# Performance work log

Measured on AMD Instinct MI355X. Metric: run time of the kernel, lower is better.

The kernel has to match this reference:

```python
import jax, jax.numpy as jnp
import numpy as np

EMBED_DIM = 1024
N_HEADS = 16
DK = EMBED_DIM // N_HEADS


def setup_inputs() -> dict:
    key = jax.random.key(0)
    ks = jax.random.split(key, 9)
    s = 1.0 / np.sqrt(EMBED_DIM)
    d = EMBED_DIM
    return {
        "x": jax.random.normal(ks[0], (2, 2048, d), dtype=jnp.float32),
        "Wq": jax.random.uniform(ks[1], (d, d), jnp.float32, -s, s),
        "bq": jax.random.uniform(ks[2], (d,), jnp.float32, -s, s),
        "Wk": jax.random.uniform(ks[3], (d, d), jnp.float32, -s, s),
        "bk": jax.random.uniform(ks[4], (d,), jnp.float32, -s, s),
        "Wv": jax.random.uniform(ks[5], (d, d), jnp.float32, -s, s),
        "bv": jax.random.uniform(ks[6], (d,), jnp.float32, -s, s),
        "Wo": jax.random.uniform(ks[7], (d, d), jnp.float32, -s, s),
        "bo": jax.random.uniform(ks[8], (d,), jnp.float32, -s, s),
    }


def reference(x, Wq, bq, Wk, bk, Wv, bv, Wo, bo):
    B, S, D = x.shape
    H, dk = N_HEADS, DK
    # QKV projections
    q = (x @ Wq + bq).reshape(B, S, H, dk).transpose(0, 2, 1, 3)  # [B,H,S,dk]
    k = (x @ Wk + bk).reshape(B, S, H, dk).transpose(0, 2, 1, 3)
    v = (x @ Wv + bv).reshape(B, S, H, dk).transpose(0, 2, 1, 3)
    # scaled dot-product attention with full score matrix (faithful to source)
    scores = jnp.einsum("bhqd,bhkd->bhqk", q, k) / jnp.sqrt(jnp.float32(dk))
    attn = jax.nn.softmax(scores, axis=-1)
    out = jnp.einsum("bhqk,bhkd->bhqd", attn, v)  # [B,H,S,dk]
    out = out.transpose(0, 2, 1, 3).reshape(B, S, D)
    return out @ Wo + bo
```

## Files before the change

### kernel.cpp

```cpp
#include <hip/hip_runtime.h>

typedef unsigned short u16;
typedef unsigned int u32;
typedef __attribute__((ext_vector_type(8))) short short8;
typedef __attribute__((ext_vector_type(4))) float float4v;

struct alignas(8) U16x4 { u16 x, y, z, w; };

__device__ __forceinline__ u16 f2b(float f) {
    union { float f; unsigned int u; } v; v.f = f;
    unsigned int r = (v.u >> 16) & 1u;
    v.u += 0x7fffu + r;
    return (u16)(v.u >> 16);
}

__device__ __forceinline__ float b2f(u16 u) {
    union { unsigned int u; float f; } v; v.u = ((u32)u) << 16; return v.f;
}

__device__ __forceinline__ void gld16(const u16* g, u16* l) {
    __builtin_amdgcn_global_load_lds(
        (const __attribute__((address_space(1))) void*)g,
        (__attribute__((address_space(3))) void*)l, 16, 0, 0);
}

__device__ __forceinline__ short8 frag8(const u16* base, int row, int cg) {
    return *(const short8*)(base + row * 64 + ((cg ^ (row & 7)) << 3));
}

__global__ __launch_bounds__(256) void prep_kernel(
    const float* __restrict__ x, const float* __restrict__ W0,
    const float* __restrict__ W1, const float* __restrict__ W2,
    const float* __restrict__ W3, u16* __restrict__ xb,
    u16* __restrict__ T0, u16* __restrict__ T1,
    u16* __restrict__ T2, u16* __restrict__ T3) {
    __shared__ float tile[32][33];
    int id = blockIdx.x;
    if (id < 4096) {
        size_t i = ((size_t)id * 256 + threadIdx.x) * 4;
        float4 v = *(const float4*)(x + i);
        U16x4 o;
        o.x = f2b(v.x); o.y = f2b(v.y); o.z = f2b(v.z); o.w = f2b(v.w);
        *(U16x4*)(xb + i) = o;
        return;
    }
    int r = id - 4096;
    int z = r >> 10, tl = r & 1023;
    const float* W = (z == 0) ? W0 : (z == 1) ? W1 : (z == 2) ? W2 : W3;
    u16* T = (z == 0) ? T0 : (z == 1) ? T1 : (z == 2) ? T2 : T3;
    int t = threadIdx.x;
    int tx = t & 31, ty = t >> 5;
    int bn = (tl & 31) * 32, bk = (tl >> 5) * 32;
#pragma unroll
    for (int p = 0; p < 4; ++p) {
        int k = ty + p * 8;
        tile[k][tx] = W[(size_t)(bk + k) * 1024 + bn + tx];
    }
    __syncthreads();
#pragma unroll
    for (int p = 0; p < 4; ++p) {
        int n = ty + p * 8;
        T[(size_t)(bn + n) * 1024 + bk + tx] = f2b(tile[tx][n]);
    }
}

__global__ __launch_bounds__(512, 2) void qkv_kernel(
    const u16* __restrict__ X,
    const u16* __restrict__ WqT, const u16* __restrict__ WkT, const u16* __restrict__ WvT,
    const float* __restrict__ bq, const float* __restrict__ bk, const float* __restrict__ bv,
    u16* __restrict__ Qo, u16* __restrict__ Ko, u16* __restrict__ VTo) {
    __shared__ __align__(16) u16 As[128 * 64];
    __shared__ __align__(16) u16 Bs[3][128 * 64];
    int id = blockIdx.x;
    int m = (id & 7) | (((id >> 3) & 3) << 3);
    int n = id >> 5;
    int t = threadIdx.x;
    int m0 = m * 128, n0 = n * 128;
    int lane = t & 63, wid = t >> 6;
    int wr = wid >> 2, wc = wid & 3;
    int l16 = lane & 15, quad = lane >> 4;
    int rl = lane >> 3, cs = lane & 7;

    int tileid = wid >> 1, half = wid & 1;
    const u16* gsrc = (tileid == 0) ? X : (tileid == 1) ? WqT
                     : (tileid == 2) ? WkT : WvT;
    int gbase = (tileid == 0) ? m0 : n0;
    u16* ldst = (tileid == 0) ? As : &Bs[tileid - 1][0];

    float4v acc[3][4][2];
    float4v zero4 = {0.f, 0.f, 0.f, 0.f};
#pragma unroll
    for (int z = 0; z < 3; ++z)
#pragma unroll
        for (int i = 0; i < 4; ++i)
#pragma unroll
            for (int j = 0; j < 2; ++j) acc[z][i][j] = zero4;

    for (int k0 = 0; k0 < 1024; k0 += 64) {
        __syncthreads();
#pragma unroll
        for (int p = 0; p < 8; ++p) {
            int q = half * 8 + p;
            int row = q * 8 + rl;
            int c = cs ^ (row & 7);
            gld16(gsrc + (size_t)(gbase + row) * 1024 + k0 + c * 8, ldst + q * 512);
        }
        __syncthreads();
#pragma unroll
        for (int ks = 0; ks < 64; ks += 32) {
            int cg = (ks >> 3) + quad;
            short8 af[4];
#pragma unroll
            for (int i = 0; i < 4; ++i)
                af[i] = frag8(As, wr * 64 + i * 16 + l16, cg);
#pragma unroll
            for (int z = 0; z < 3; ++z) {
                short8 bf[2];
#pragma unroll
                for (int j = 0; j < 2; ++j)
                    bf[j] = frag8(&Bs[z][0], wc * 32 + j * 16 + l16, cg);
#pragma unroll
                for (int i = 0; i < 4; ++i)
#pragma unroll
                    for (int j = 0; j < 2; ++j)
                        acc[z][i][j] = __builtin_amdgcn_mfma_f32_16x16x32_bf16(
                            af[i], bf[j], acc[z][i][j], 0, 0, 0);
            }
        }
    }

    const float QSCALE = 0.18033688011112042f;
#pragma unroll
    for (int j = 0; j < 2; ++j) {
        int n1 = n0 + wc * 32 + j * 16 + l16;
        float bql = bq[n1], bkl = bk[n1], bvl = bv[n1];
#pragma unroll
        for (int i = 0; i < 4; ++i) {
            int mbase = m0 + wr * 64 + i * 16 + quad * 4;
#pragma unroll
            for (int r = 0; r < 4; ++r) {
                Qo[(size_t)(mbase + r) * 1024 + n1] =
                    f2b((acc[0][i][j][r] + bql) * QSCALE);
                Ko[(size_t)(mbase + r) * 1024 + n1] =
                    f2b(acc[1][i][j][r] + bkl);
            }
            int bidx = mbase >> 11, s = mbase & 2047;
            size_t base =
                ((size_t)((bidx * 16 + (n1 >> 6)) * 64 + (n1 & 63))) * 2048 + s;
            U16x4 pk;
            pk.x = f2b(acc[2][i][j][0] + bvl);
            pk.y = f2b(acc[2][i][j][1] + bvl);
            pk.z = f2b(acc[2][i][j][2] + bvl);
            pk.w = f2b(acc[2][i][j][3] + bvl);
            *(U16x4*)(VTo + base) = pk;
        }
    }
}

__global__ __launch_bounds__(256) void oproj_kernel(const u16* __restrict__ X,
                                                    const u16* __restrict__ WoT,
                                                    const float* __restrict__ bias,
                                                    float* __restrict__ out) {
    __shared__ __align__(16) u16 As[64 * 64];
    __shared__ __align__(16) u16 Bs[128 * 64];
    int id = blockIdx.x;
    int m = (id & 7) | (((id >> 3) & 7) << 3);
    int n = id >> 6;
    int t = threadIdx.x;
    int m0 = m * 64, n0 = n * 128;
    int lane = t & 63, wid = t >> 6;
    int l16 = lane & 15, quad = lane >> 4;
    int rl = lane >> 3, cs = lane & 7;

    float4v acc[4][2];
    float4v zero4 = {0.f, 0.f, 0.f, 0.f};
#pragma unroll
    for (int i = 0; i < 4; ++i)
#pragma unroll
        for (int j = 0; j < 2; ++j) acc[i][j] = zero4;

    for (int k0 = 0; k0 < 1024; k0 += 64) {
        __syncthreads();
#pragma unroll
        for (int p = 0; p < 2; ++p) {
            int blk = wid * 2 + p;
            int row = blk * 8 + rl;
            int c = cs ^ (row & 7);
            gld16(X + (size_t)(m0 + row) * 1024 + k0 + c * 8, As + blk * 512);
        }
#pragma unroll
        for (int p = 0; p < 4; ++p) {
            int blk = wid * 4 + p;
            int row = blk * 8 + rl;
            int c = cs ^ (row & 7);
            gld16(WoT + (size_t)(n0 + row) * 1024 + k0 + c * 8, Bs + blk * 512);
        }
        __syncthreads();
#pragma unroll
        for (int ks = 0; ks < 64; ks += 32) {
            int cg = (ks >> 3) + quad;
            short8 af[4], bf[2];
#pragma unroll
            for (int i = 0; i < 4; ++i) af[i] = frag8(As, i * 16 + l16, cg);
#pragma unroll
            for (int j = 0; j < 2; ++j) bf[j] = frag8(Bs, wid * 32 + j * 16 + l16, cg);
#pragma unroll
            for (int i = 0; i < 4; ++i)
#pragma unroll
                for (int j = 0; j < 2; ++j)
                    acc[i][j] = __builtin_amdgcn_mfma_f32_16x16x32_bf16(
                        af[i], bf[j], acc[i][j], 0, 0, 0);
        }
    }

#pragma unroll
    for (int j = 0; j < 2; ++j) {
        int n1 = n0 + wid * 32 + j * 16 + l16;
        float bvl = bias[n1];
#pragma unroll
        for (int i = 0; i < 4; ++i) {
            int mbase = m0 + i * 16 + quad * 4;
#pragma unroll
            for (int r = 0; r < 4; ++r)
                out[(size_t)(mbase + r) * 1024 + n1] = acc[i][j][r] + bvl;
        }
    }
}

__global__ __launch_bounds__(128, 2) void flash_kernel(const u16* __restrict__ Q,
                                                       const u16* __restrict__ Kn,
                                                       const u16* __restrict__ VT,
                                                       u16* __restrict__ Opart,
                                                       float* __restrict__ lpart) {
    __shared__ __align__(16) u16 Ks[64 * 64];
    __shared__ __align__(16) u16 Vs[64 * 64];
    __shared__ __align__(16) u16 Ps[128][72];

    int id = blockIdx.x;
    int bh = (id & 7) | (((id >> 3) & 3) << 3);
    int rest = id >> 5;
    int qb = rest & 15, kvz = rest >> 4;
    int b = bh >> 4, h = bh & 15;
    int t = threadIdx.x;
    int wid = t >> 6, lane = t & 63;
    int l16 = lane & 15, quad = lane >> 4;
    int rl = lane >> 3, cs = lane & 7;
    int q0 = qb * 128 + wid * 64;
    size_t kbase = (size_t)(b * 2048) * 1024 + h * 64;
    size_t vbase = (size_t)(bh * 64) * 2048;

    short8 qf[4][2];
#pragma unroll
    for (int j = 0; j < 4; ++j)
#pragma unroll
        for (int kk = 0; kk < 2; ++kk)
            qf[j][kk] = *(const short8*)(
                Q + ((size_t)(b * 2048 + q0 + j * 16 + l16)) * 1024 + h * 64 +
                kk * 32 + quad * 8);

    float4v oacc[4][4];
    float lreg[4];
    float4v zero4 = {0.f, 0.f, 0.f, 0.f};
#pragma unroll
    for (int ip = 0; ip < 4; ++ip) {
        lreg[ip] = 0.f;
#pragma unroll
        for (int jd = 0; jd < 4; ++jd) oacc[ip][jd] = zero4;
    }

    for (int kvi = 0; kvi < 16; ++kvi) {
        int kv = kvz * 1024 + kvi * 64;
        __syncthreads();
        if (wid == 0) {
#pragma unroll
            for (int p = 0; p < 8; ++p) {
                int row = p * 8 + rl;
                int c = cs ^ (row & 7);
                gld16(Kn + kbase + (size_t)(kv + row) * 1024 + c * 8, Ks + p * 512);
            }
        } else {
#pragma unroll
            for (int p = 0; p < 8; ++p) {
                int row = p * 8 + rl;
                int c = cs ^ (row & 7);
                gld16(VT + vbase + (size_t)row * 2048 + kv + c * 8, Vs + p * 512);
            }
        }
        __syncthreads();

#pragma unroll
        for (int i = 0; i < 4; ++i) {
            float4v sacc[4];
#pragma unroll
            for (int j = 0; j < 4; ++j) sacc[j] = zero4;
#pragma unroll
            for (int kk = 0; kk < 2; ++kk) {
                short8 kf = frag8(Ks, i * 16 + l16, kk * 4 + quad);
#pragma unroll
                for (int j = 0; j < 4; ++j)
                    sacc[j] = __builtin_amdgcn_mfma_f32_16x16x32_bf16(
                        kf, qf[j][kk], sacc[j], 0, 0, 0);
            }
#pragma unroll
            for (int j = 0; j < 4; ++j) {
                float e0f = __builtin_amdgcn_exp2f(sacc[j][0]);
                float e1f = __builtin_amdgcn_exp2f(sacc[j][1]);
                float e2f = __builtin_amdgcn_exp2f(sacc[j][2]);
                float e3f = __builtin_amdgcn_exp2f(sacc[j][3]);
                lreg[j] += (e0f + e1f) + (e2f + e3f);
                u32 e0 = __float_as_uint(e0f) + 0x8000u;
                u32 e1 = __float_as_uint(e1f) + 0x8000u;
                u32 e2 = __float_as_uint(e2f) + 0x8000u;
                u32 e3 = __float_as_uint(e3f) + 0x8000u;
                uint2 pk;
                pk.x = __builtin_amdgcn_perm(e1, e0, 0x07060302u);
                pk.y = __builtin_amdgcn_perm(e3, e2, 0x07060302u);
                *(uint2*)(&Ps[wid * 64 + j * 16 + l16][i * 16 + quad * 4]) = pk;
            }
        }

#pragma unroll
        for (int kk = 0; kk < 2; ++kk) {
            int cg = kk * 4 + quad;
            short8 pf[4];
#pragma unroll
            for (int ip = 0; ip < 4; ++ip)
                pf[ip] = *(const short8*)(
                    &Ps[wid * 64 + ip * 16 + l16][kk * 32 + quad * 8]);
#pragma unroll
            for (int jd = 0; jd < 4; ++jd) {
                short8 vf = frag8(Vs, jd * 16 + l16, cg);
#pragma unroll
                for (int ip = 0; ip < 4; ++ip)
                    oacc[ip][jd] = __builtin_amdgcn_mfma_f32_16x16x32_bf16(
                        pf[ip], vf, oacc[ip][jd], 0, 0, 0);
            }
        }
    }

#pragma unroll
    for (int j = 0; j < 4; ++j) {
        lreg[j] += __shfl_xor(lreg[j], 16);
        lreg[j] += __shfl_xor(lreg[j], 32);
    }

    size_t obase = (size_t)kvz * 4194304;
#pragma unroll
    for (int ip = 0; ip < 4; ++ip)
#pragma unroll
        for (int r = 0; r < 4; ++r) {
            int q = q0 + ip * 16 + quad * 4 + r;
#pragma unroll
            for (int jd = 0; jd < 4; ++jd)
                Opart[obase + ((size_t)(b * 2048 + q)) * 1024 + h * 64 +
                      jd * 16 + l16] = f2b(oacc[ip][jd][r]);
        }
    if (quad == 0) {
#pragma unroll
        for (int j = 0; j < 4; ++j) {
            int q = q0 + j * 16 + l16;
            lpart[kvz * 65536 + (b * 2048 + q) * 16 + h] = lreg[j];
        }
    }
}

__global__ __launch_bounds__(256) void combine_kernel(const u16* __restrict__ Op,
                                                      const float* __restrict__ lp,
                                                      u16* __restrict__ out) {
    int idx = blockIdx.x * 256 + threadIdx.x;
    size_t i = (size_t)idx * 4;
    int qg = idx >> 8;
    int d = (idx & 255) * 4;
    int h = d >> 6;
    float l0 = lp[qg * 16 + h], l1 = lp[65536 + qg * 16 + h];
    float inv = 1.0f / (l0 + l1);
    U16x4 o0 = *(const U16x4*)(Op + i);
    U16x4 o1 = *(const U16x4*)(Op + 4194304 + i);
    U16x4 o;
    o.x = f2b((b2f(o0.x) + b2f(o1.x)) * inv);
    o.y = f2b((b2f(o0.y) + b2f(o1.y)) * inv);
    o.z = f2b((b2f(o0.z) + b2f(o1.z)) * inv);
    o.w = f2b((b2f(o0.w) + b2f(o1.w)) * inv);
    *(U16x4*)(out + i) = o;
}

extern "C" void kernel_launch(void* const* d_in, const int* in_sizes, int n_in,
                              void* d_out, int out_size, void* d_ws, size_t ws_size,
                              hipStream_t stream) {
    const float* x  = (const float*)d_in[0];
    const float* Wq = (const float*)d_in[1];
    const float* bq = (const float*)d_in[2];
    const float* Wk = (const float*)d_in[3];
    const float* bk = (const float*)d_in[4];
    const float* Wv = (const float*)d_in[5];
    const float* bv = (const float*)d_in[6];
    const float* Wo = (const float*)d_in[7];
    const float* bo = (const float*)d_in[8];
    float* out = (float*)d_out;

    char* ws = (char*)d_ws;
    const size_t MB = 1024 * 1024;
    u16* xb  = (u16*)(ws);
    u16* wqt = (u16*)(ws + 8 * MB);
    u16* wkt = (u16*)(ws + 10 * MB);
    u16* wvt = (u16*)(ws + 12 * MB);
    u16* wot = (u16*)(ws + 14 * MB);
    u16* qb_ = (u16*)(ws + 16 * MB);
    u16* kb_ = (u16*)(ws + 24 * MB);
    u16* vt_ = (u16*)(ws + 32 * MB);
    u16* ab_ = (u16*)(ws + 40 * MB);
    u16* op_ = (u16*)(ws + 48 * MB);
    float* lp_ = (float*)(ws + 64 * MB);

    prep_kernel<<<8192, 256, 0, stream>>>(x, Wq, Wk, Wv, Wo, xb,
                                          wqt, wkt, wvt, wot);
    qkv_kernel<<<256, 512, 0, stream>>>(xb, wqt, wkt, wvt, bq, bk, bv,
                                        qb_, kb_, vt_);
    flash_kernel<<<1024, 128, 0, stream>>>(qb_, kb_, vt_, op_, lp_);
    combine_kernel<<<4096, 256, 0, stream>>>(op_, lp_, ab_);
    oproj_kernel<<<512, 256, 0, stream>>>(ab_, wot, bo, out);
}
```

Baseline: 191.2 us.

## Double-buffer K/V tiles in flash kernel with 4-wave blocks and swizzled P

The flash attention kernel now uses 256-thread blocks that cover 256 query rows, so one K/V tile in LDS serves four waves instead of two. K/V tiles are double-buffered: all waves issue async global-to-LDS loads for the next tile before computing on the current one, which removes the second barrier per iteration. The P scratch buffer moves from a padded layout to an XOR-swizzled layout read through the shared fragment helper, and s_setprio is raised around the MFMA sections. The cost is more LDS per block, which may limit occupancy, and correctness depends on the async loads completing before the next barrier.

```diff
diff --git a/kernel.cpp b/kernel.cpp
--- a/kernel.cpp
+++ b/kernel.cpp
@@ -227,27 +227,28 @@
     }
 }
 
-__global__ __launch_bounds__(128, 2) void flash_kernel(const u16* __restrict__ Q,
+__global__ __launch_bounds__(256, 2) void flash_kernel(const u16* __restrict__ Q,
                                                        const u16* __restrict__ Kn,
                                                        const u16* __restrict__ VT,
                                                        u16* __restrict__ Opart,
                                                        float* __restrict__ lpart) {
-    __shared__ __align__(16) u16 Ks[64 * 64];
-    __shared__ __align__(16) u16 Vs[64 * 64];
-    __shared__ __align__(16) u16 Ps[128][72];
+    __shared__ __align__(16) u16 Ks[2][64 * 64];
+    __shared__ __align__(16) u16 Vs[2][64 * 64];
+    __shared__ __align__(16) u16 Ps[256 * 64];
 
     int id = blockIdx.x;
     int bh = (id & 7) | (((id >> 3) & 3) << 3);
     int rest = id >> 5;
-    int qb = rest & 15, kvz = rest >> 4;
+    int qb = rest & 7, kvz = rest >> 3;
     int b = bh >> 4, h = bh & 15;
     int t = threadIdx.x;
     int wid = t >> 6, lane = t & 63;
     int l16 = lane & 15, quad = lane >> 4;
     int rl = lane >> 3, cs = lane & 7;
-    int q0 = qb * 128 + wid * 64;
+    int q0 = qb * 256 + wid * 64;
     size_t kbase = (size_t)(b * 2048) * 1024 + h * 64;
     size_t vbase = (size_t)(bh * 64) * 2048;
+    int kv0 = kvz * 1024;
 
     short8 qf[4][2];
 #pragma unroll
@@ -268,39 +269,41 @@
         for (int jd = 0; jd < 4; ++jd) oacc[ip][jd] = zero4;
     }
 
+#define STAGE_KV(buf, kv)                                                     \
+    {                                                                         \
+        _Pragma("unroll") for (int p2 = 0; p2 < 2; ++p2) {                    \
+            int p = wid * 2 + p2;                                             \
+            int row = p * 8 + rl;                                             \
+            int c = cs ^ (row & 7);                                           \
+            gld16(Kn + kbase + (size_t)((kv) + row) * 1024 + c * 8,           \
+                  &Ks[buf][p * 512]);                                         \
+            gld16(VT + vbase + (size_t)row * 2048 + (kv) + c * 8,             \
+                  &Vs[buf][p * 512]);                                         \
+        }                                                                     \
+    }
+
+    STAGE_KV(0, kv0);
+
     for (int kvi = 0; kvi < 16; ++kvi) {
-        int kv = kvz * 1024 + kvi * 64;
+        int buf = kvi & 1;
         __syncthreads();
-        if (wid == 0) {
-#pragma unroll
-            for (int p = 0; p < 8; ++p) {
-                int row = p * 8 + rl;
-                int c = cs ^ (row & 7);
-                gld16(Kn + kbase + (size_t)(kv + row) * 1024 + c * 8, Ks + p * 512);
-            }
-        } else {
-#pragma unroll
-            for (int p = 0; p < 8; ++p) {
-                int row = p * 8 + rl;
-                int c = cs ^ (row & 7);
-                gld16(VT + vbase + (size_t)row * 2048 + kv + c * 8, Vs + p * 512);
-            }
-        }
-        __syncthreads();
+        if (kvi + 1 < 16) STAGE_KV(buf ^ 1, kv0 + (kvi + 1) * 64);
 
 #pragma unroll
         for (int i = 0; i < 4; ++i) {
             float4v sacc[4];
 #pragma unroll
             for (int j = 0; j < 4; ++j) sacc[j] = zero4;
+            __builtin_amdgcn_s_setprio(1);
 #pragma unroll
             for (int kk = 0; kk < 2; ++kk) {
-                short8 kf = frag8(Ks, i * 16 + l16, kk * 4 + quad);
+                short8 kf = frag8(&Ks[buf][0], i * 16 + l16, kk * 4 + quad);
 #pragma unroll
                 for (int j = 0; j < 4; ++j)
                     sacc[j] = __builtin_amdgcn_mfma_f32_16x16x32_bf16(
                         kf, qf[j][kk], sacc[j], 0, 0, 0);
             }
+            __builtin_amdgcn_s_setprio(0);
 #pragma unroll
             for (int j = 0; j < 4; ++j) {
                 float e0f = __builtin_amdgcn_exp2f(sacc[j][0]);
@@ -315,28 +318,33 @@
                 uint2 pk;
                 pk.x = __builtin_amdgcn_perm(e1, e0, 0x07060302u);
                 pk.y = __builtin_amdgcn_perm(e3, e2, 0x07060302u);
-                *(uint2*)(&Ps[wid * 64 + j * 16 + l16][i * 16 + quad * 4]) = pk;
+                int prow = wid * 64 + j * 16 + l16;
+                *(uint2*)(Ps + prow * 64 +
+                          (((i * 2 + (quad >> 1)) ^ (prow & 7)) << 3) +
+                          ((quad & 1) << 2)) = pk;
             }
         }
 
+        __builtin_amdgcn_s_setprio(1);
 #pragma unroll
         for (int kk = 0; kk < 2; ++kk) {
             int cg = kk * 4 + quad;
             short8 pf[4];
 #pragma unroll
             for (int ip = 0; ip < 4; ++ip)
-                pf[ip] = *(const short8*)(
-                    &Ps[wid * 64 + ip * 16 + l16][kk * 32 + quad * 8]);
+                pf[ip] = frag8(Ps, wid * 64 + ip * 16 + l16, cg);
 #pragma unroll
             for (int jd = 0; jd < 4; ++jd) {
-                short8 vf = frag8(Vs, jd * 16 + l16, cg);
+                short8 vf = frag8(&Vs[buf][0], jd * 16 + l16, cg);
 #pragma unroll
                 for (int ip = 0; ip < 4; ++ip)
                     oacc[ip][jd] = __builtin_amdgcn_mfma_f32_16x16x32_bf16(
                         pf[ip], vf, oacc[ip][jd], 0, 0, 0);
             }
         }
-    }
+        __builtin_amdgcn_s_setprio(0);
+    }
+#undef STAGE_KV
 
 #pragma unroll
     for (int j = 0; j < 4; ++j) {
@@ -416,7 +424,7 @@
                                           wqt, wkt, wvt, wot);
     qkv_kernel<<<256, 512, 0, stream>>>(xb, wqt, wkt, wvt, bq, bk, bv,
                                         qb_, kb_, vt_);
-    flash_kernel<<<1024, 128, 0, stream>>>(qb_, kb_, vt_, op_, lp_);
+    flash_kernel<<<512, 256, 0, stream>>>(qb_, kb_, vt_, op_, lp_);
     combine_kernel<<<4096, 256, 0, stream>>>(op_, lp_, ab_);
     oproj_kernel<<<512, 256, 0, stream>>>(ab_, wot, bo, out);
 }
```

Result: no change. 193.5 us (+1.2%).
